# Kernel optimization log

Hardware: AMD Instinct MI355X
Metric: run time of the kernel (lower is better)

## Reference

```python
import jax, jax.numpy as jnp
import numpy as np


def _pairwise_dist(e, c):
    # Euclidean distance matrix [N, K], matching torch.cdist(p=2)
    e2 = jnp.sum(e * e, axis=1, keepdims=True)          # [N, 1]
    c2 = jnp.sum(c * c, axis=1)[None, :]                # [1, K]
    d2 = e2 + c2 - 2.0 * (e @ c.T)                      # [N, K]
    return jnp.sqrt(jnp.maximum(d2, 0.0))


def setup_inputs() -> dict:
    key = jax.random.key(0)
    k1, k2 = jax.random.split(key)
    N, K, D = 262144, 1024, 128
    embeddings = jax.random.normal(k1, (N, D), dtype=jnp.float32)
    cluster_centroids = jax.random.normal(k2, (K, D), dtype=jnp.float32)
    return {"embeddings": embeddings, "cluster_centroids": cluster_centroids}


def reference(embeddings, cluster_centroids):
    dist = _pairwise_dist(embeddings, cluster_centroids)   # [N, K]
    labels = jnp.argmin(dist, axis=1)                      # [N]
    logits = -dist
    # CrossEntropyLoss(mean): logsumexp(logits) - logits[label]
    # logits[label] = -min(dist) since label is the argmin
    lse = jax.nn.logsumexp(logits, axis=1)                 # [N]
    target_logit = -jnp.min(dist, axis=1)                  # [N]
    loss = jnp.mean(lse - target_logit)
    return (loss, labels)
```

## Files before the change

### kernel.cpp

```cpp
#include <hip/hip_runtime.h>
#include <stdint.h>

#define D_DIM 128
#define K_DIM 1024
#define BM 64
#define N_TOTAL 262144
#define MAXF 16384
#define RR 16

#define SIGMA 2.0813689810056077f
#define NS2   (-2.0f * SIGMA)
#define TAUS  (0.1f * SIGMA)
#define LN2   0.69314718055994531f

#if __has_builtin(__builtin_amdgcn_exp2f)
#define EXP2F __builtin_amdgcn_exp2f
#else
#define EXP2F exp2f
#endif

typedef __attribute__((ext_vector_type(8))) short short8;
typedef __attribute__((ext_vector_type(4))) float f32x4;

__device__ __forceinline__ unsigned short f2bf(float f) {
    union { float f; uint32_t u; } v; v.f = f;
    uint32_t r = v.u + 0x7fffu + ((v.u >> 16) & 1u);
    return (unsigned short)(r >> 16);
}
__device__ __forceinline__ float bf2f(unsigned short h) {
    union { float f; uint32_t u; } v; v.u = ((uint32_t)h) << 16;
    return v.f;
}

__global__ void prep_c2_kernel(const float* __restrict__ C,
                               float* __restrict__ c2) {
    int col = blockIdx.x * blockDim.x + threadIdx.x;
    if (col >= K_DIM) return;
    const float4* C4 = (const float4*)(C + (size_t)col * D_DIM);
    float s0 = 0.f, s1 = 0.f, s2 = 0.f, s3 = 0.f;
    #pragma unroll
    for (int dq = 0; dq < 32; ++dq) {
        float4 v = C4[dq];
        s0 = fmaf(v.x, v.x, s0);
        s1 = fmaf(v.y, v.y, s1);
        s2 = fmaf(v.z, v.z, s2);
        s3 = fmaf(v.w, v.w, s3);
    }
    c2[col] = (s0 + s1) + (s2 + s3);
}

__global__ void prep_frag_kernel(const float* __restrict__ C,
                                 unsigned short* __restrict__ Cfrag) {
    int g = blockIdx.x * blockDim.x + threadIdx.x;
    int col = g >> 5;
    int dq = g & 31;
    float4 v = ((const float4*)C)[g];
    unsigned short h0 = f2bf(v.x), h1 = f2bf(v.y), h2 = f2bf(v.z), h3 = f2bf(v.w);
    unsigned short l0 = f2bf(v.x - bf2f(h0)), l1 = f2bf(v.y - bf2f(h1));
    unsigned short l2 = f2bf(v.z - bf2f(h2)), l3 = f2bf(v.w - bf2f(h3));
    int ntg = col >> 4;
    int cl = col & 15;
    int d0 = dq << 2;
    int ds = d0 >> 5;
    int lane = (((d0 >> 3) & 3) << 4) | cl;
    int jb = d0 & 7;
    size_t idx = (((size_t)(ntg * 4 + ds) * 64 + lane) * 8 + jb);
    uint2 hv = make_uint2((uint32_t)h0 | ((uint32_t)h1 << 16),
                          (uint32_t)h2 | ((uint32_t)h3 << 16));
    uint2 lv = make_uint2((uint32_t)l0 | ((uint32_t)l1 << 16),
                          (uint32_t)l2 | ((uint32_t)l3 << 16));
    *(uint2*)&Cfrag[idx] = hv;
    *(uint2*)&Cfrag[131072 + idx] = lv;
}

__global__ __launch_bounds__(256, 3) void fused_mfma_kernel(
        const float* __restrict__ E,
        const unsigned short* __restrict__ Cfrag,
        const float* __restrict__ c2g,
        float* __restrict__ out,
        int* __restrict__ fcnt,
        int* __restrict__ flist)
{
    __shared__ unsigned short Elds[32 * 528];
    __shared__ float c2s[K_DIM];
    __shared__ float e2s[BM];
    __shared__ uint32_t mrgk[BM * 2];
    __shared__ uint32_t mrgm[BM * 2];
    __shared__ float    mrgs[BM * 2];

    const int tid = threadIdx.x;
    const int lane = tid & 63;
    const int w = tid >> 6;
    const int Rh = w >> 1;
    const int Nh = w & 1;
    const int q = lane >> 4;
    const int mcol = lane & 15;
    const int row0 = blockIdx.x * BM;

    for (int i = tid; i < K_DIM; i += 256) c2s[i] = SIGMA * c2g[i];

    {
        const float4* E4 = (const float4*)(E + (size_t)row0 * D_DIM);
        #pragma unroll
        for (int it = 0; it < 8; ++it) {
            int chunk = it * 256 + tid;
            int r = chunk >> 5;
            int dq = chunk & 31;
            float4 v = E4[chunk];
            float p = fmaf(v.x, v.x, fmaf(v.y, v.y, fmaf(v.z, v.z, v.w * v.w)));
            #pragma unroll
            for (int off = 1; off < 32; off <<= 1) p += __shfl_xor(p, off);
            if ((tid & 31) == 0) e2s[r] = p;
            unsigned short h0 = f2bf(v.x), h1 = f2bf(v.y), h2 = f2bf(v.z), h3 = f2bf(v.w);
            unsigned short l0 = f2bf(v.x - bf2f(h0)), l1 = f2bf(v.y - bf2f(h1));
            unsigned short l2 = f2bf(v.z - bf2f(h2)), l3 = f2bf(v.w - bf2f(h3));
            int d0 = dq << 2;
            int mt = r >> 4;
            int ds = d0 >> 5;
            int lane_slot = (((d0 >> 3) & 3) << 4) | (r & 15);
            int jb = d0 & 7;
            int segh = (mt * 4 + ds) * 528 + lane_slot * 8 + jb;
            uint2 hv = make_uint2((uint32_t)h0 | ((uint32_t)h1 << 16),
                                  (uint32_t)h2 | ((uint32_t)h3 << 16));
            uint2 lv = make_uint2((uint32_t)l0 | ((uint32_t)l1 << 16),
                                  (uint32_t)l2 | ((uint32_t)l3 << 16));
            *(uint2*)&Elds[segh] = hv;
            *(uint2*)&Elds[16 * 528 + segh] = lv;
        }
    }
    __syncthreads();

    float e2rs[8];
    #pragma unroll
    for (int s = 0; s < 8; ++s)
        e2rs[s] = SIGMA * e2s[(Rh * 2 + (s >> 2)) * 16 + q * 4 + (s & 3)];

    uint32_t k1v[8], m2v[8];
    float sv[8];
    #pragma unroll
    for (int s = 0; s < 8; ++s) { k1v[s] = 0xFFFFFFFFu; m2v[s] = 0xFFFFFFFFu; sv[s] = 0.f; }

    const short8* Bfrag = (const short8*)Cfrag;

    #pragma unroll 1
    for (int kc = 0; kc < 16; ++kc) {
        f32x4 acc[2][2];
        #pragma unroll
        for (int i = 0; i < 2; ++i)
            #pragma unroll
            for (int j = 0; j < 2; ++j)
                acc[i][j] = (f32x4){0.f, 0.f, 0.f, 0.f};

        #pragma unroll
        for (int ds = 0; ds < 4; ++ds) {
            short8 ah[2], al[2];
            #pragma unroll
            for (int mi = 0; mi < 2; ++mi) {
                int seg = ((Rh * 2 + mi) * 4 + ds) * 528 + lane * 8;
                ah[mi] = *(const short8*)&Elds[seg];
                al[mi] = *(const short8*)&Elds[16 * 528 + seg];
            }
            #pragma unroll
            for (int ni = 0; ni < 2; ++ni) {
                int ntg = kc * 4 + Nh * 2 + ni;
                size_t bidx = ((size_t)ntg * 4 + ds) * 64 + lane;
                short8 bh = Bfrag[bidx];
                short8 bl = Bfrag[16384 + bidx];
                #pragma unroll
                for (int mi = 0; mi < 2; ++mi) {
                    acc[mi][ni] = __builtin_amdgcn_mfma_f32_16x16x32_bf16(al[mi], bh, acc[mi][ni], 0, 0, 0);
                    acc[mi][ni] = __builtin_amdgcn_mfma_f32_16x16x32_bf16(ah[mi], bl, acc[mi][ni], 0, 0, 0);
                    acc[mi][ni] = __builtin_amdgcn_mfma_f32_16x16x32_bf16(ah[mi], bh, acc[mi][ni], 0, 0, 0);
                }
            }
        }
        #pragma unroll
        for (int ni = 0; ni < 2; ++ni) {
            int kidx = kc * 64 + Nh * 32 + ni * 16 + mcol;
            float c2v = c2s[kidx];
            #pragma unroll
            for (int mi = 0; mi < 2; ++mi) {
                #pragma unroll
                for (int r = 0; r < 4; ++r) {
                    int s = mi * 4 + r;
                    float d2 = fmaf(NS2, acc[mi][ni][r], e2rs[s] + c2v);
                    uint32_t key = (__float_as_uint(d2) & 0xFFFFFC00u) | (uint32_t)kidx;
                    float dist = __builtin_amdgcn_sqrtf(__builtin_fabsf(d2));
                    sv[s] += EXP2F(-dist);
                    uint32_t k1 = k1v[s];
                    m2v[s] = min(m2v[s], max(k1, key));
                    k1v[s] = min(k1, key);
                }
            }
        }
    }

    #pragma unroll
    for (int s = 0; s < 8; ++s) {
        #pragma unroll
        for (int off = 1; off < 16; off <<= 1) {
            uint32_t ok1 = __shfl_xor(k1v[s], off);
            uint32_t om2 = __shfl_xor(m2v[s], off);
            float osv = __shfl_xor(sv[s], off);
            m2v[s] = min(min(m2v[s], om2), max(k1v[s], ok1));
            k1v[s] = min(k1v[s], ok1);
            sv[s] += osv;
        }
    }
    if (mcol == 0) {
        #pragma unroll
        for (int s = 0; s < 8; ++s) {
            int row = (Rh * 2 + (s >> 2)) * 16 + q * 4 + (s & 3);
            mrgk[row * 2 + Nh] = k1v[s];
            mrgm[row * 2 + Nh] = m2v[s];
            mrgs[row * 2 + Nh] = sv[s];
        }
    }
    __syncthreads();

    if (tid < BM) {
        uint32_t ka = mrgk[tid * 2 + 0], kb = mrgk[tid * 2 + 1];
        uint32_t ma = mrgm[tid * 2 + 0], mb = mrgm[tid * 2 + 1];
        float ss = mrgs[tid * 2 + 0] + mrgs[tid * 2 + 1];
        uint32_t k1 = min(ka, kb);
        uint32_t m2 = min(min(ma, mb), max(ka, kb));
        float m1q = __uint_as_float(k1 & 0xFFFFFC00u);
        float m2q = __uint_as_float(m2 & 0xFFFFFC00u);
        int i1 = (int)(k1 & 1023u);
        float lossr = logf(ss) + sqrtf(m1q) * LN2;
        out[1 + row0 + tid] = (float)i1;
        if (m2q - m1q < TAUS) {
            int idx = atomicAdd(fcnt, 1);
            if (idx < MAXF) flist[idx] = row0 + tid;
        }
        float v = lossr;
        #pragma unroll
        for (int off = 32; off > 0; off >>= 1) v += __shfl_down(v, off);
        if (tid == 0) atomicAdd(out, v * (1.0f / (float)N_TOTAL));
    }
}

__global__ void refine_kernel(const float* __restrict__ E,
                              const float* __restrict__ C,
                              const float* __restrict__ c2g,
                              const int* __restrict__ fcnt,
                              const int* __restrict__ flist,
                              float* __restrict__ out) {
    int cnt = *fcnt;
    if (cnt > MAXF) cnt = MAXF;
    int base = blockIdx.x * RR;
    if (base >= cnt) return;

    __shared__ float Er[RR][D_DIM];
    __shared__ float e2r_[RR];
    __shared__ int rowid[RR];
    __shared__ unsigned long long wred[RR][4];

    const int tid = threadIdx.x;
    if (tid < RR) {
        int rr = base + tid;
        if (rr >= cnt) rr = cnt - 1;
        rowid[tid] = flist[rr];
    }
    __syncthreads();
    for (int i = tid; i < RR * 32; i += 256) {
        int rr = i >> 5, dq = i & 31;
        ((float4*)Er[rr])[dq] = ((const float4*)(E + (size_t)rowid[rr] * D_DIM))[dq];
    }
    __syncthreads();
    if (tid < RR) {
        float s = 0.f;
        for (int d = 0; d < D_DIM; ++d) s = fmaf(Er[tid][d], Er[tid][d], s);
        e2r_[tid] = s;
    }
    __syncthreads();

    unsigned long long best[RR];
    #pragma unroll
    for (int r = 0; r < RR; ++r) best[r] = ~0ull;

    for (int ii = 0; ii < 4; ++ii) {
        int k = ii * 256 + tid;
        const float4* C4 = (const float4*)(C + (size_t)k * D_DIM);
        float dot[RR];
        #pragma unroll
        for (int r = 0; r < RR; ++r) dot[r] = 0.f;
        for (int dq = 0; dq < 32; ++dq) {
            float4 cv = C4[dq];
            int d0 = dq * 4;
            #pragma unroll
            for (int r = 0; r < RR; ++r) {
                dot[r] = fmaf(Er[r][d0], cv.x,
                          fmaf(Er[r][d0 + 1], cv.y,
                           fmaf(Er[r][d0 + 2], cv.z,
                            fmaf(Er[r][d0 + 3], cv.w, dot[r]))));
            }
        }
        float c2v = c2g[k];
        #pragma unroll
        for (int r = 0; r < RR; ++r) {
            float d2 = (e2r_[r] + c2v) - 2.f * dot[r];
            float dist = sqrtf(fmaxf(d2, 0.f));
            unsigned long long key =
                (((unsigned long long)__float_as_uint(dist)) << 10) | (unsigned)k;
            best[r] = best[r] < key ? best[r] : key;
        }
    }

    const int wv = tid >> 6;
    #pragma unroll
    for (int r = 0; r < RR; ++r) {
        unsigned long long b = best[r];
        #pragma unroll
        for (int off = 32; off > 0; off >>= 1) {
            unsigned long long o = __shfl_xor(b, off);
            b = o < b ? o : b;
        }
        if ((tid & 63) == 0) wred[r][wv] = b;
    }
    __syncthreads();
    if (tid < RR) {
        unsigned long long b = wred[tid][0];
        #pragma unroll
        for (int j = 1; j < 4; ++j) b = wred[tid][j] < b ? wred[tid][j] : b;
        out[1 + rowid[tid]] = (float)(int)(b & 1023u);
    }
}

extern "C" void kernel_launch(void* const* d_in, const int* in_sizes, int n_in,
                              void* d_out, int out_size, void* d_ws, size_t ws_size,
                              hipStream_t stream) {
    const float* E = (const float*)d_in[0];
    const float* C = (const float*)d_in[1];
    float* out = (float*)d_out;

    unsigned short* Cfrag = (unsigned short*)d_ws;
    float* c2 = (float*)((char*)d_ws + 524288);
    int* fcnt = (int*)((char*)d_ws + 524288 + 4096);
    int* flist = fcnt + 1;

    hipMemsetAsync(d_out, 0, sizeof(float), stream);
    hipMemsetAsync(fcnt, 0, sizeof(int), stream);

    prep_c2_kernel<<<dim3(16), dim3(64), 0, stream>>>(C, c2);
    prep_frag_kernel<<<dim3(128), dim3(256), 0, stream>>>(C, Cfrag);
    fused_mfma_kernel<<<dim3(N_TOTAL / BM), dim3(256), 0, stream>>>(E, Cfrag, c2, out, fcnt, flist);
    refine_kernel<<<dim3(MAXF / RR), dim3(256), 0, stream>>>(E, C, c2, fcnt, flist, out);
}
```

Before: 470.7 us.

## Restructure fallback refinement loop and raise MFMA wave priority

The exact-fp32 fallback kernel for ambiguous rows now processes 8 rows per block instead of 16. It accumulates dot products for all four centroid groups in a single pass over D, loading each row chunk from LDS as a float4 once per dq and reusing it across the four centroids. The main MFMA loop is wrapped in s_setprio(1)/s_setprio(0) so waves issuing matrix instructions get scheduling priority. Halving RR doubles the fallback block count and the re-reading of centroids, while the 8x4 accumulator array raises register use.

```diff
diff --git a/kernel.cpp b/kernel.cpp
--- a/kernel.cpp
+++ b/kernel.cpp
@@ -6,7 +6,7 @@
 #define BM 64
 #define N_TOTAL 262144
 #define MAXF 16384
-#define RR 16
+#define RR 8
 
 #define SIGMA 2.0813689810056077f
 #define NS2   (-2.0f * SIGMA)
@@ -151,6 +151,7 @@
             for (int j = 0; j < 2; ++j)
                 acc[i][j] = (f32x4){0.f, 0.f, 0.f, 0.f};
 
+        __builtin_amdgcn_s_setprio(1);
         #pragma unroll
         for (int ds = 0; ds < 4; ++ds) {
             short8 ah[2], al[2];
@@ -174,6 +175,8 @@
                 }
             }
         }
+        __builtin_amdgcn_s_setprio(0);
+
         #pragma unroll
         for (int ni = 0; ni < 2; ++ni) {
             int kidx = kc * 64 + Nh * 32 + ni * 16 + mcol;
@@ -275,31 +278,45 @@
     }
     __syncthreads();
 
+    const float4* C4b[4];
+    #pragma unroll
+    for (int ii = 0; ii < 4; ++ii)
+        C4b[ii] = (const float4*)(C + (size_t)(ii * 256 + tid) * D_DIM);
+
+    float dot[RR][4];
+    #pragma unroll
+    for (int r = 0; r < RR; ++r)
+        #pragma unroll
+        for (int ii = 0; ii < 4; ++ii) dot[r][ii] = 0.f;
+
+    for (int dq = 0; dq < 32; ++dq) {
+        float4 er[RR];
+        #pragma unroll
+        for (int r = 0; r < RR; ++r) er[r] = ((const float4*)Er[r])[dq];
+        #pragma unroll
+        for (int ii = 0; ii < 4; ++ii) {
+            float4 cv = C4b[ii][dq];
+            #pragma unroll
+            for (int r = 0; r < RR; ++r) {
+                dot[r][ii] = fmaf(er[r].x, cv.x,
+                              fmaf(er[r].y, cv.y,
+                               fmaf(er[r].z, cv.z,
+                                fmaf(er[r].w, cv.w, dot[r][ii]))));
+            }
+        }
+    }
+
     unsigned long long best[RR];
     #pragma unroll
     for (int r = 0; r < RR; ++r) best[r] = ~0ull;
 
+    #pragma unroll
     for (int ii = 0; ii < 4; ++ii) {
         int k = ii * 256 + tid;
-        const float4* C4 = (const float4*)(C + (size_t)k * D_DIM);
-        float dot[RR];
-        #pragma unroll
-        for (int r = 0; r < RR; ++r) dot[r] = 0.f;
-        for (int dq = 0; dq < 32; ++dq) {
-            float4 cv = C4[dq];
-            int d0 = dq * 4;
-            #pragma unroll
-            for (int r = 0; r < RR; ++r) {
-                dot[r] = fmaf(Er[r][d0], cv.x,
-                          fmaf(Er[r][d0 + 1], cv.y,
-                           fmaf(Er[r][d0 + 2], cv.z,
-                            fmaf(Er[r][d0 + 3], cv.w, dot[r]))));
-            }
-        }
         float c2v = c2g[k];
         #pragma unroll
         for (int r = 0; r < RR; ++r) {
-            float d2 = (e2r_[r] + c2v) - 2.f * dot[r];
+            float d2 = (e2r_[r] + c2v) - 2.f * dot[r][ii];
             float dist = sqrtf(fmaxf(d2, 0.f));
             unsigned long long key =
                 (((unsigned long long)__float_as_uint(dist)) << 10) | (unsigned)k;
```

Measured after the change: 496.2 us. 1.05x slower.
